# Optimization experiments

Hardware: AMD Instinct MI355X
Metric: run time of the kernel (lower is better)

The kernel has to match this reference:

```python
import jax, jax.numpy as jnp
import numpy as np

N = 50000
E = 800000
IN, H, OUT = 128, 96, 64
BN_EPS = 1e-5


def setup_inputs() -> dict:
    key = jax.random.key(0)
    ks = jax.random.split(key, 16)
    x = jax.random.normal(ks[0], (N, IN), dtype=jnp.float32)
    edge_index = jax.random.randint(ks[1], (2, E), 0, N, dtype=jnp.int64)
    edge_weight = jax.random.uniform(ks[2], (E,), dtype=jnp.float32)
    def lin(k, fo, fi):
        # PyG glorot-ish init
        s = 1.0 / np.sqrt(fi)
        return jax.random.uniform(k, (fo, fi), minval=-s, maxval=s, dtype=jnp.float32)
    W1, b1 = lin(ks[3], H, IN), jnp.zeros((H,), jnp.float32)
    W2, b2 = lin(ks[4], H, H), jnp.zeros((H,), jnp.float32)
    W3, b3 = lin(ks[5], OUT, H), jnp.zeros((OUT,), jnp.float32)
    g1 = jnp.ones((H,), jnp.float32); beta1 = jnp.zeros((H,), jnp.float32)
    m1 = 0.1 * jax.random.normal(ks[6], (H,), dtype=jnp.float32)
    v1 = jnp.abs(1.0 + 0.1 * jax.random.normal(ks[7], (H,), dtype=jnp.float32))
    g2 = jnp.ones((H,), jnp.float32); beta2 = jnp.zeros((H,), jnp.float32)
    m2 = 0.1 * jax.random.normal(ks[8], (H,), dtype=jnp.float32)
    v2 = jnp.abs(1.0 + 0.1 * jax.random.normal(ks[9], (H,), dtype=jnp.float32))
    return dict(x=x, edge_index=edge_index, edge_weight=edge_weight,
                W1=W1, b1=b1, W2=W2, b2=b2, W3=W3, b3=b3,
                g1=g1, beta1=beta1, m1=m1, v1=v1,
                g2=g2, beta2=beta2, m2=m2, v2=v2)


def gcn_norm(edge_index, edge_weight, n):
    # PyG gcn_norm with add_self_loops=True, fill_value=1.0
    loop = jnp.arange(n, dtype=edge_index.dtype)
    row = jnp.concatenate([edge_index[0], loop])  # sources
    col = jnp.concatenate([edge_index[1], loop])  # targets
    ew = jnp.concatenate([edge_weight, jnp.ones((n,), edge_weight.dtype)])
    deg = jax.ops.segment_sum(ew, col, num_segments=n)
    dis = jnp.where(deg > 0, jax.lax.rsqrt(deg), 0.0)  # inf -> 0 masked_fill
    norm = dis[row] * ew * dis[col]
    return row, col, norm


def gcn_conv(x, row, col, norm, W, b, n):
    xw = x @ W.T                       # [N, F_out] dense transform first
    msg = norm[:, None] * xw[row]      # [E+N, F_out] gather + edge scale
    out = jax.ops.segment_sum(msg, col, num_segments=n)  # scatter-add
    return out + b


def bn_eval(x, gamma, beta, mean, var):
    return (x - mean) * jax.lax.rsqrt(var + BN_EPS) * gamma + beta


def reference(x, edge_index, edge_weight, W1, b1, W2, b2, W3, b3,
              g1, beta1, m1, v1, g2, beta2, m2, v2):
    n = x.shape[0]
    row, col, norm = gcn_norm(edge_index, edge_weight, n)  # cached=True: shared
    h = gcn_conv(x, row, col, norm, W1, b1, n)
    h = jax.nn.relu(bn_eval(h, g1, beta1, m1, v1))
    h = gcn_conv(h, row, col, norm, W2, b2, n)
    h = jax.nn.relu(bn_eval(h, g2, beta2, m2, v2))
    out = gcn_conv(h, row, col, norm, W3, b3, n)
    return out
```

## Files before the change

### kernel.cpp

```cpp
#include <hip/hip_runtime.h>
#include <hip/hip_fp16.h>


constexpr float BN_EPS = 1e-5f;
constexpr float FIXED_SCALE = 33554432.0f;
constexpr float INV_FIXED_SCALE = 1.0f / 33554432.0f;
constexpr float NORM_SCALE = 32768.0f;
constexpr float INV_NORM_SCALE = 1.0f / 32768.0f;

typedef _Float16 f16x8 __attribute__((ext_vector_type(8)));
typedef float f32x4 __attribute__((ext_vector_type(4)));


template <int K, int F, bool F32X, bool F32W>
__device__ __forceinline__ void gemm_body(const void* __restrict__ Xin,
                                          const void* __restrict__ Win,
                                          _Float16* __restrict__ Y, int n,
                                          int bid, int tid) {
    constexpr int KT = K / 32;
    constexpr int FT = F / 16;
    int wave = tid >> 6;
    int lane = tid & 63;
    int n0 = (bid * 4 + wave) * 16;
    if (n0 >= n) return;
    int quad = lane >> 4;
    int r = lane & 15;

    f16x8 a[KT];
    if (F32X) {
        const float* xr = (const float*)Xin + (size_t)(n0 + r) * K + quad * 8;
#pragma unroll
        for (int kt = 0; kt < KT; ++kt) {
            float4 v0 = *(const float4*)(xr + kt * 32);
            float4 v1 = *(const float4*)(xr + kt * 32 + 4);
            f16x8 t = {(_Float16)v0.x, (_Float16)v0.y, (_Float16)v0.z, (_Float16)v0.w,
                       (_Float16)v1.x, (_Float16)v1.y, (_Float16)v1.z, (_Float16)v1.w};
            a[kt] = t;
        }
    } else {
        const f16x8* xr = (const f16x8*)((const _Float16*)Xin + (size_t)(n0 + r) * K + quad * 8);
#pragma unroll
        for (int kt = 0; kt < KT; ++kt) a[kt] = xr[kt * 4];
    }

    f32x4 acc[FT];
#pragma unroll
    for (int ft = 0; ft < FT; ++ft) acc[ft] = (f32x4){0.f, 0.f, 0.f, 0.f};

#pragma unroll
    for (int kt = 0; kt < KT; ++kt) {
#pragma unroll
        for (int ft = 0; ft < FT; ++ft) {
            f16x8 b;
            if (F32W) {
                const float* wr = (const float*)Win + (size_t)(ft * 16 + r) * K + kt * 32 + quad * 8;
                float4 v0 = *(const float4*)wr;
                float4 v1 = *(const float4*)(wr + 4);
                f16x8 t = {(_Float16)v0.x, (_Float16)v0.y, (_Float16)v0.z, (_Float16)v0.w,
                           (_Float16)v1.x, (_Float16)v1.y, (_Float16)v1.z, (_Float16)v1.w};
                b = t;
            } else {
                b = *(const f16x8*)((const _Float16*)Win + (size_t)(ft * 16 + r) * K + kt * 32 + quad * 8);
            }
            acc[ft] = __builtin_amdgcn_mfma_f32_16x16x32_f16(a[kt], b, acc[ft], 0, 0, 0);
        }
    }

#pragma unroll
    for (int ft = 0; ft < FT; ++ft) {
#pragma unroll
        for (int reg = 0; reg < 4; ++reg) {
            int row = n0 + quad * 4 + reg;
            Y[(size_t)row * F + ft * 16 + r] = (_Float16)acc[ft][reg];
        }
    }
}

template <int K, int F>
__global__ __launch_bounds__(256) void k_gemm(const _Float16* __restrict__ X,
                                              const _Float16* __restrict__ Wh,
                                              _Float16* __restrict__ Y, int n) {
    gemm_body<K, F, false, false>(X, Wh, Y, n, blockIdx.x, threadIdx.x);
}


__global__ __launch_bounds__(256) void k_mega(
    const int* __restrict__ col_idx, const float* __restrict__ ew,
    unsigned long long* packed, int* rank, int e_cnt, int deg_b,
    const float* __restrict__ x, const float* __restrict__ W1,
    _Float16* __restrict__ bufA, int n, int gg,
    const float* __restrict__ W2, const float* __restrict__ W3,
    _Float16* __restrict__ w2h, _Float16* __restrict__ w3h,
    int w2n4, int w3n4) {
    int b = blockIdx.x;
    if (b < deg_b) {
        int e = b * 256 + threadIdx.x;
        if (e < e_cnt) {
            int c = col_idx[e];
            unsigned int wfix = (unsigned int)(ew[e] * FIXED_SCALE + 0.5f);
            unsigned long long inc = (1ull << 32) | (unsigned long long)wfix;
            unsigned long long old = atomicAdd(&packed[c], inc);
            rank[e] = (int)(old >> 32);
        }
    } else if (b < deg_b + gg) {
        gemm_body<128, 96, true, true>(x, W1, bufA, n, b - deg_b, threadIdx.x);
    } else {
        int i = (b - deg_b - gg) * 256 + threadIdx.x;
        const float* src;
        _Float16* dst;
        int off;
        if (i < w2n4) { src = W2; dst = w2h; off = i; }
        else if (i < w2n4 + w3n4) { src = W3; dst = w3h; off = i - w2n4; }
        else return;
        float4 v = ((const float4*)src)[off];
        __half2 h0 = __floats2half2_rn(v.x, v.y);
        __half2 h1 = __floats2half2_rn(v.z, v.w);
        *(uint2*)(dst + (size_t)off * 4) = make_uint2(*(unsigned*)&h0, *(unsigned*)&h1);
    }
}


__global__ void k_scan1(const unsigned long long* __restrict__ packed,
                        int* bsum, float* dis, int n) {
    __shared__ int s[256];
    int i = blockIdx.x * 256 + threadIdx.x;
    int cnt = 0;
    if (i < n) {
        unsigned long long p = packed[i];
        cnt = (int)(p >> 32);
        float wsum = (float)(unsigned int)(p & 0xffffffffull) * INV_FIXED_SCALE;
        dis[i] = rsqrtf(1.0f + wsum);
    }
    s[threadIdx.x] = cnt;
    __syncthreads();
    for (int off = 128; off > 0; off >>= 1) {
        if (threadIdx.x < off) s[threadIdx.x] += s[threadIdx.x + off];
        __syncthreads();
    }
    if (threadIdx.x == 0) bsum[blockIdx.x] = s[0];
}

__global__ void k_scan23(const unsigned long long* __restrict__ packed,
                         const int* __restrict__ bsum,
                         int* row_ptr, int n, int e_total, int nb) {
    __shared__ int sb[256];
    __shared__ int s[256];
    int t = threadIdx.x;
    int bv = (t < nb) ? bsum[t] : 0;
    sb[t] = bv;
    __syncthreads();
    for (int off = 1; off < 256; off <<= 1) {
        int x = (t >= off) ? sb[t - off] : 0;
        __syncthreads();
        sb[t] += x;
        __syncthreads();
    }
    int boff = (blockIdx.x == 0) ? 0 : sb[blockIdx.x - 1];

    int i = blockIdx.x * 256 + t;
    int v = (i < n) ? (int)(packed[i] >> 32) : 0;
    s[t] = v;
    __syncthreads();
    for (int off = 1; off < 256; off <<= 1) {
        int x = (t >= off) ? s[t - off] : 0;
        __syncthreads();
        s[t] += x;
        __syncthreads();
    }
    int ex = s[t] - v + boff;
    if (i < n) row_ptr[i] = ex;
    if (i == 0) row_ptr[n] = e_total;
}

__global__ void k_fill(const int* __restrict__ row_idx, const int* __restrict__ col_idx,
                       const float* __restrict__ ew, const float* __restrict__ dis,
                       const int* __restrict__ row_ptr, const int* __restrict__ rank,
                       unsigned* ep, int e_cnt) {
    int e = blockIdx.x * 256 + threadIdx.x;
    if (e < e_cnt) {
        int r = row_idx[e];
        int c = col_idx[e];
        float nm = dis[r] * ew[e] * dis[c];
        unsigned q = (unsigned)(nm * NORM_SCALE + 0.5f);
        if (q > 65535u) q = 65535u;
        int p = row_ptr[c] + rank[e];
        ep[p] = ((unsigned)r << 16) | q;
    }
}


__device__ inline void h8_acc(uint4 u, float w, float acc[8]) {
    float2 a = __half22float2(*(const __half2*)&u.x);
    float2 b = __half22float2(*(const __half2*)&u.y);
    float2 c = __half22float2(*(const __half2*)&u.z);
    float2 d = __half22float2(*(const __half2*)&u.w);
    acc[0] = fmaf(w, a.x, acc[0]); acc[1] = fmaf(w, a.y, acc[1]);
    acc[2] = fmaf(w, b.x, acc[2]); acc[3] = fmaf(w, b.y, acc[3]);
    acc[4] = fmaf(w, c.x, acc[4]); acc[5] = fmaf(w, c.y, acc[5]);
    acc[6] = fmaf(w, d.x, acc[6]); acc[7] = fmaf(w, d.y, acc[7]);
}

template <int F, bool BN, bool F32OUT>
__global__ __launch_bounds__(256) void k_aggr(
    const _Float16* __restrict__ xw, const int* __restrict__ row_ptr,
    const unsigned* __restrict__ ep,
    const float* __restrict__ dis, const float* __restrict__ bias,
    const float* __restrict__ g, const float* __restrict__ beta,
    const float* __restrict__ m, const float* __restrict__ v,
    void* __restrict__ out, int n) {
    constexpr int FQ = F / 8;
    int tg = blockIdx.x * 256 + threadIdx.x;
    int node = tg / FQ;
    int q = tg - node * FQ;
    if (node >= n) return;

    const uint4* __restrict__ base = (const uint4*)xw;

    float acc[8];
    {
        float d = dis[node];
        float d2 = d * d;
        uint4 sv = base[(size_t)node * FQ + q];
        float t[8];
        h8_acc(sv, d2, (float*)memset(t, 0, sizeof(t)));
#pragma unroll
        for (int j = 0; j < 8; ++j) acc[j] = t[j];
    }

    int e0 = row_ptr[node], e1 = row_ptr[node + 1];
    int e = e0;
    for (; e + 4 <= e1; e += 4) {
        unsigned p0 = ep[e + 0], p1 = ep[e + 1], p2 = ep[e + 2], p3 = ep[e + 3];
        uint4 x0 = base[(size_t)(p0 >> 16) * FQ + q];
        uint4 x1 = base[(size_t)(p1 >> 16) * FQ + q];
        uint4 x2 = base[(size_t)(p2 >> 16) * FQ + q];
        uint4 x3 = base[(size_t)(p3 >> 16) * FQ + q];
        h8_acc(x0, (float)(p0 & 0xffffu) * INV_NORM_SCALE, acc);
        h8_acc(x1, (float)(p1 & 0xffffu) * INV_NORM_SCALE, acc);
        h8_acc(x2, (float)(p2 & 0xffffu) * INV_NORM_SCALE, acc);
        h8_acc(x3, (float)(p3 & 0xffffu) * INV_NORM_SCALE, acc);
    }
    for (; e < e1; ++e) {
        unsigned p = ep[e];
        uint4 xv = base[(size_t)(p >> 16) * FQ + q];
        h8_acc(xv, (float)(p & 0xffffu) * INV_NORM_SCALE, acc);
    }

    int fb = q * 8;
    const float4* bb = (const float4*)(bias + fb);
    float4 b0 = bb[0], b1 = bb[1];
    acc[0] += b0.x; acc[1] += b0.y; acc[2] += b0.z; acc[3] += b0.w;
    acc[4] += b1.x; acc[5] += b1.y; acc[6] += b1.z; acc[7] += b1.w;
    if (BN) {
        const float* gp = g + fb;
        const float* bp = beta + fb;
        const float* mp = m + fb;
        const float* vp = v + fb;
#pragma unroll
        for (int j = 0; j < 8; ++j) {
            acc[j] = fmaxf((acc[j] - mp[j]) * rsqrtf(vp[j] + BN_EPS) * gp[j] + bp[j], 0.f);
        }
    }
    if (F32OUT) {
        float* op = (float*)out + (size_t)node * F + fb;
        *(float4*)(op + 0) = make_float4(acc[0], acc[1], acc[2], acc[3]);
        *(float4*)(op + 4) = make_float4(acc[4], acc[5], acc[6], acc[7]);
    } else {
        __half2 h0 = __floats2half2_rn(acc[0], acc[1]);
        __half2 h1 = __floats2half2_rn(acc[2], acc[3]);
        __half2 h2 = __floats2half2_rn(acc[4], acc[5]);
        __half2 h3 = __floats2half2_rn(acc[6], acc[7]);
        uint4 u = make_uint4(*(unsigned*)&h0, *(unsigned*)&h1,
                             *(unsigned*)&h2, *(unsigned*)&h3);
        ((uint4*)out)[(size_t)node * FQ + q] = u;
    }
}


extern "C" void kernel_launch(void* const* d_in, const int* in_sizes, int n_in,
                              void* d_out, int out_size, void* d_ws, size_t ws_size,
                              hipStream_t stream) {
    constexpr int IN = 128, H = 96, OUT = 64;

    const float* x   = (const float*)d_in[0];
    const int*   ei  = (const int*)d_in[1];
    const float* ew  = (const float*)d_in[2];
    const float* W1  = (const float*)d_in[3];
    const float* b1  = (const float*)d_in[4];
    const float* W2  = (const float*)d_in[5];
    const float* b2  = (const float*)d_in[6];
    const float* W3  = (const float*)d_in[7];
    const float* b3  = (const float*)d_in[8];
    const float* g1  = (const float*)d_in[9];
    const float* be1 = (const float*)d_in[10];
    const float* m1  = (const float*)d_in[11];
    const float* v1  = (const float*)d_in[12];
    const float* g2  = (const float*)d_in[13];
    const float* be2 = (const float*)d_in[14];
    const float* m2  = (const float*)d_in[15];
    const float* v2  = (const float*)d_in[16];

    const int N = in_sizes[0] / IN;
    const int E = in_sizes[2];
    const int* row_idx = ei;
    const int* col_idx = ei + E;

    char* ws = (char*)d_ws;
    size_t off = 0;
    auto alloc = [&](size_t bytes) -> void* {
        void* p = ws + off;
        off = (off + bytes + 255) & ~(size_t)255;
        return p;
    };
    unsigned long long* packed = (unsigned long long*)alloc((size_t)N * 8);
    float*     dis     = (float*)alloc((size_t)N * 4);
    int*       row_ptr = (int*)alloc((size_t)(N + 1) * 4);
    int*       bsum    = (int*)alloc(256 * 4);
    int*       rank    = (int*)alloc((size_t)E * 4);
    unsigned*  ep      = (unsigned*)alloc((size_t)E * 4);
    _Float16*  w2h     = (_Float16*)alloc((size_t)H * H * 2);
    _Float16*  w3h     = (_Float16*)alloc((size_t)OUT * H * 2);
    _Float16*  bufA    = (_Float16*)alloc((size_t)N * H * 2);
    _Float16*  bufB    = (_Float16*)alloc((size_t)N * H * 2);
    (void)ws_size; (void)n_in; (void)out_size;

    constexpr int W2N4 = H * H / 4, W3N4 = OUT * H / 4;
    const int NB = (N + 255) / 256;
    const int DEG_B = (E + 255) / 256;
    const int GG = (N / 16 + 3) / 4;
    const int CVT_B = (W2N4 + W3N4 + 255) / 256;

    hipMemsetAsync(packed, 0, (size_t)N * 8, stream);
    k_mega<<<DEG_B + GG + CVT_B, 256, 0, stream>>>(
        col_idx, ew, packed, rank, E, DEG_B,
        x, W1, bufA, N, GG, W2, W3, w2h, w3h, W2N4, W3N4);
    k_scan1<<<NB, 256, 0, stream>>>(packed, bsum, dis, N);
    k_scan23<<<NB, 256, 0, stream>>>(packed, bsum, row_ptr, N, E, NB);
    k_fill<<<DEG_B, 256, 0, stream>>>(row_idx, col_idx, ew, dis, row_ptr, rank, ep, E);

    const int GA96 = ((size_t)N * (H / 8) + 255) / 256;
    const int GA64 = ((size_t)N * (OUT / 8) + 255) / 256;

    k_aggr<H, true, false><<<GA96, 256, 0, stream>>>(
        bufA, row_ptr, ep, dis, b1, g1, be1, m1, v1, bufB, N);

    k_gemm<H, H><<<GG, 256, 0, stream>>>(bufB, w2h, bufA, N);
    k_aggr<H, true, false><<<GA96, 256, 0, stream>>>(
        bufA, row_ptr, ep, dis, b2, g2, be2, m2, v2, bufB, N);

    k_gemm<H, OUT><<<GG, 256, 0, stream>>>(bufB, w3h, bufA, N);
    k_aggr<OUT, false, true><<<GA64, 256, 0, stream>>>(
        bufA, row_ptr, ep, dis, b3, nullptr, nullptr, nullptr, nullptr, d_out, N);
}
```

Measured before the change: 281.4 us.

## Fuse all GCN stages into one persistent cooperative kernel with grid syncs

```diff
diff --git a/kernel.cpp b/kernel.cpp
--- a/kernel.cpp
+++ b/kernel.cpp
@@ -1,5 +1,8 @@
 #include <hip/hip_runtime.h>
 #include <hip/hip_fp16.h>
+#include <hip/hip_cooperative_groups.h>
+
+namespace cg = cooperative_groups;
 
 
 constexpr float BN_EPS = 1e-5f;
@@ -11,17 +14,28 @@
 typedef _Float16 f16x8 __attribute__((ext_vector_type(8)));
 typedef float f32x4 __attribute__((ext_vector_type(4)));
 
+struct P {
+    const int* col_idx; const int* row_idx; const float* ew;
+    const float* x; const float* W1; const float* W2; const float* W3;
+    const float* b1; const float* g1; const float* be1; const float* m1; const float* v1;
+    const float* b2; const float* g2; const float* be2; const float* m2; const float* v2;
+    const float* b3;
+    unsigned long long* packed;
+    int* rank; int* row_ptr; int* bsum;
+    float* dis; unsigned* ep;
+    _Float16* w2h; _Float16* w3h; _Float16* bufA; _Float16* bufB;
+    float* out;
+    int N, E, NB;
+};
+
 
 template <int K, int F, bool F32X, bool F32W>
-__device__ __forceinline__ void gemm_body(const void* __restrict__ Xin,
+__device__ __forceinline__ void gemm_wave(const void* __restrict__ Xin,
                                           const void* __restrict__ Win,
-                                          _Float16* __restrict__ Y, int n,
-                                          int bid, int tid) {
+                                          _Float16* __restrict__ Y,
+                                          int n0, int lane, int n) {
     constexpr int KT = K / 32;
     constexpr int FT = F / 16;
-    int wave = tid >> 6;
-    int lane = tid & 63;
-    int n0 = (bid * 4 + wave) * 16;
     if (n0 >= n) return;
     int quad = lane >> 4;
     int r = lane & 15;
@@ -76,118 +90,14 @@
     }
 }
 
-template <int K, int F>
-__global__ __launch_bounds__(256) void k_gemm(const _Float16* __restrict__ X,
-                                              const _Float16* __restrict__ Wh,
-                                              _Float16* __restrict__ Y, int n) {
-    gemm_body<K, F, false, false>(X, Wh, Y, n, blockIdx.x, threadIdx.x);
-}
-
-
-__global__ __launch_bounds__(256) void k_mega(
-    const int* __restrict__ col_idx, const float* __restrict__ ew,
-    unsigned long long* packed, int* rank, int e_cnt, int deg_b,
-    const float* __restrict__ x, const float* __restrict__ W1,
-    _Float16* __restrict__ bufA, int n, int gg,
-    const float* __restrict__ W2, const float* __restrict__ W3,
-    _Float16* __restrict__ w2h, _Float16* __restrict__ w3h,
-    int w2n4, int w3n4) {
-    int b = blockIdx.x;
-    if (b < deg_b) {
-        int e = b * 256 + threadIdx.x;
-        if (e < e_cnt) {
-            int c = col_idx[e];
-            unsigned int wfix = (unsigned int)(ew[e] * FIXED_SCALE + 0.5f);
-            unsigned long long inc = (1ull << 32) | (unsigned long long)wfix;
-            unsigned long long old = atomicAdd(&packed[c], inc);
-            rank[e] = (int)(old >> 32);
-        }
-    } else if (b < deg_b + gg) {
-        gemm_body<128, 96, true, true>(x, W1, bufA, n, b - deg_b, threadIdx.x);
-    } else {
-        int i = (b - deg_b - gg) * 256 + threadIdx.x;
-        const float* src;
-        _Float16* dst;
-        int off;
-        if (i < w2n4) { src = W2; dst = w2h; off = i; }
-        else if (i < w2n4 + w3n4) { src = W3; dst = w3h; off = i - w2n4; }
-        else return;
-        float4 v = ((const float4*)src)[off];
-        __half2 h0 = __floats2half2_rn(v.x, v.y);
-        __half2 h1 = __floats2half2_rn(v.z, v.w);
-        *(uint2*)(dst + (size_t)off * 4) = make_uint2(*(unsigned*)&h0, *(unsigned*)&h1);
-    }
-}
-
-
-__global__ void k_scan1(const unsigned long long* __restrict__ packed,
-                        int* bsum, float* dis, int n) {
-    __shared__ int s[256];
-    int i = blockIdx.x * 256 + threadIdx.x;
-    int cnt = 0;
-    if (i < n) {
-        unsigned long long p = packed[i];
-        cnt = (int)(p >> 32);
-        float wsum = (float)(unsigned int)(p & 0xffffffffull) * INV_FIXED_SCALE;
-        dis[i] = rsqrtf(1.0f + wsum);
-    }
-    s[threadIdx.x] = cnt;
-    __syncthreads();
-    for (int off = 128; off > 0; off >>= 1) {
-        if (threadIdx.x < off) s[threadIdx.x] += s[threadIdx.x + off];
-        __syncthreads();
-    }
-    if (threadIdx.x == 0) bsum[blockIdx.x] = s[0];
-}
-
-__global__ void k_scan23(const unsigned long long* __restrict__ packed,
-                         const int* __restrict__ bsum,
-                         int* row_ptr, int n, int e_total, int nb) {
-    __shared__ int sb[256];
-    __shared__ int s[256];
-    int t = threadIdx.x;
-    int bv = (t < nb) ? bsum[t] : 0;
-    sb[t] = bv;
-    __syncthreads();
-    for (int off = 1; off < 256; off <<= 1) {
-        int x = (t >= off) ? sb[t - off] : 0;
-        __syncthreads();
-        sb[t] += x;
-        __syncthreads();
-    }
-    int boff = (blockIdx.x == 0) ? 0 : sb[blockIdx.x - 1];
-
-    int i = blockIdx.x * 256 + t;
-    int v = (i < n) ? (int)(packed[i] >> 32) : 0;
-    s[t] = v;
-    __syncthreads();
-    for (int off = 1; off < 256; off <<= 1) {
-        int x = (t >= off) ? s[t - off] : 0;
-        __syncthreads();
-        s[t] += x;
-        __syncthreads();
-    }
-    int ex = s[t] - v + boff;
-    if (i < n) row_ptr[i] = ex;
-    if (i == 0) row_ptr[n] = e_total;
-}
-
-__global__ void k_fill(const int* __restrict__ row_idx, const int* __restrict__ col_idx,
-                       const float* __restrict__ ew, const float* __restrict__ dis,
-                       const int* __restrict__ row_ptr, const int* __restrict__ rank,
-                       unsigned* ep, int e_cnt) {
-    int e = blockIdx.x * 256 + threadIdx.x;
-    if (e < e_cnt) {
-        int r = row_idx[e];
-        int c = col_idx[e];
-        float nm = dis[r] * ew[e] * dis[c];
-        unsigned q = (unsigned)(nm * NORM_SCALE + 0.5f);
-        if (q > 65535u) q = 65535u;
-        int p = row_ptr[c] + rank[e];
-        ep[p] = ((unsigned)r << 16) | q;
-    }
-}
-
+
+__device__ inline void cvt8(uint4 u, float* f) {
+    float2 t;
+    t = __half22float2(*(const __half2*)&u.x); f[0] = t.x; f[1] = t.y;
+    t = __half22float2(*(const __half2*)&u.y); f[2] = t.x; f[3] = t.y;
+    t = __half22float2(*(const __half2*)&u.z); f[4] = t.x; f[5] = t.y;
+    t = __half22float2(*(const __half2*)&u.w); f[6] = t.x; f[7] = t.y;
+}
 
 __device__ inline void h8_acc(uint4 u, float w, float acc[8]) {
     float2 a = __half22float2(*(const __half2*)&u.x);
@@ -201,79 +111,198 @@
 }
 
 template <int F, bool BN, bool F32OUT>
-__global__ __launch_bounds__(256) void k_aggr(
-    const _Float16* __restrict__ xw, const int* __restrict__ row_ptr,
-    const unsigned* __restrict__ ep,
-    const float* __restrict__ dis, const float* __restrict__ bias,
-    const float* __restrict__ g, const float* __restrict__ beta,
-    const float* __restrict__ m, const float* __restrict__ v,
-    void* __restrict__ out, int n) {
+__device__ void aggr_phase(const _Float16* __restrict__ xw,
+                           const int* __restrict__ row_ptr,
+                           const unsigned* __restrict__ ep,
+                           const float* __restrict__ dis,
+                           const float* __restrict__ bias,
+                           const float* __restrict__ g, const float* __restrict__ beta,
+                           const float* __restrict__ m, const float* __restrict__ v,
+                           void* __restrict__ out, int n, int tid, int gsz) {
     constexpr int FQ = F / 8;
-    int tg = blockIdx.x * 256 + threadIdx.x;
-    int node = tg / FQ;
-    int q = tg - node * FQ;
-    if (node >= n) return;
-
     const uint4* __restrict__ base = (const uint4*)xw;
-
-    float acc[8];
-    {
-        float d = dis[node];
-        float d2 = d * d;
-        uint4 sv = base[(size_t)node * FQ + q];
-        float t[8];
-        h8_acc(sv, d2, (float*)memset(t, 0, sizeof(t)));
-#pragma unroll
-        for (int j = 0; j < 8; ++j) acc[j] = t[j];
-    }
-
-    int e0 = row_ptr[node], e1 = row_ptr[node + 1];
-    int e = e0;
-    for (; e + 4 <= e1; e += 4) {
-        unsigned p0 = ep[e + 0], p1 = ep[e + 1], p2 = ep[e + 2], p3 = ep[e + 3];
-        uint4 x0 = base[(size_t)(p0 >> 16) * FQ + q];
-        uint4 x1 = base[(size_t)(p1 >> 16) * FQ + q];
-        uint4 x2 = base[(size_t)(p2 >> 16) * FQ + q];
-        uint4 x3 = base[(size_t)(p3 >> 16) * FQ + q];
-        h8_acc(x0, (float)(p0 & 0xffffu) * INV_NORM_SCALE, acc);
-        h8_acc(x1, (float)(p1 & 0xffffu) * INV_NORM_SCALE, acc);
-        h8_acc(x2, (float)(p2 & 0xffffu) * INV_NORM_SCALE, acc);
-        h8_acc(x3, (float)(p3 & 0xffffu) * INV_NORM_SCALE, acc);
-    }
-    for (; e < e1; ++e) {
-        unsigned p = ep[e];
-        uint4 xv = base[(size_t)(p >> 16) * FQ + q];
-        h8_acc(xv, (float)(p & 0xffffu) * INV_NORM_SCALE, acc);
-    }
-
-    int fb = q * 8;
-    const float4* bb = (const float4*)(bias + fb);
-    float4 b0 = bb[0], b1 = bb[1];
-    acc[0] += b0.x; acc[1] += b0.y; acc[2] += b0.z; acc[3] += b0.w;
-    acc[4] += b1.x; acc[5] += b1.y; acc[6] += b1.z; acc[7] += b1.w;
-    if (BN) {
-        const float* gp = g + fb;
-        const float* bp = beta + fb;
-        const float* mp = m + fb;
-        const float* vp = v + fb;
-#pragma unroll
-        for (int j = 0; j < 8; ++j) {
-            acc[j] = fmaxf((acc[j] - mp[j]) * rsqrtf(vp[j] + BN_EPS) * gp[j] + bp[j], 0.f);
-        }
-    }
-    if (F32OUT) {
-        float* op = (float*)out + (size_t)node * F + fb;
-        *(float4*)(op + 0) = make_float4(acc[0], acc[1], acc[2], acc[3]);
-        *(float4*)(op + 4) = make_float4(acc[4], acc[5], acc[6], acc[7]);
+    int total = n * FQ;
+    for (int it = tid; it < total; it += gsz) {
+        int node = it / FQ;
+        int q = it - node * FQ;
+
+        float acc[8];
+        {
+            float d = dis[node];
+            float d2 = d * d;
+            uint4 sv = base[(size_t)node * FQ + q];
+            float t[8];
+            cvt8(sv, t);
+#pragma unroll
+            for (int j = 0; j < 8; ++j) acc[j] = d2 * t[j];
+        }
+
+        int e0 = row_ptr[node], e1 = row_ptr[node + 1];
+        int e = e0;
+        for (; e + 4 <= e1; e += 4) {
+            unsigned p0 = ep[e + 0], p1 = ep[e + 1], p2 = ep[e + 2], p3 = ep[e + 3];
+            uint4 x0 = base[(size_t)(p0 >> 16) * FQ + q];
+            uint4 x1 = base[(size_t)(p1 >> 16) * FQ + q];
+            uint4 x2 = base[(size_t)(p2 >> 16) * FQ + q];
+            uint4 x3 = base[(size_t)(p3 >> 16) * FQ + q];
+            h8_acc(x0, (float)(p0 & 0xffffu) * INV_NORM_SCALE, acc);
+            h8_acc(x1, (float)(p1 & 0xffffu) * INV_NORM_SCALE, acc);
+            h8_acc(x2, (float)(p2 & 0xffffu) * INV_NORM_SCALE, acc);
+            h8_acc(x3, (float)(p3 & 0xffffu) * INV_NORM_SCALE, acc);
+        }
+        for (; e < e1; ++e) {
+            unsigned p = ep[e];
+            uint4 xv = base[(size_t)(p >> 16) * FQ + q];
+            h8_acc(xv, (float)(p & 0xffffu) * INV_NORM_SCALE, acc);
+        }
+
+        int fb = q * 8;
+        const float4* bb = (const float4*)(bias + fb);
+        float4 b0 = bb[0], b1 = bb[1];
+        acc[0] += b0.x; acc[1] += b0.y; acc[2] += b0.z; acc[3] += b0.w;
+        acc[4] += b1.x; acc[5] += b1.y; acc[6] += b1.z; acc[7] += b1.w;
+        if (BN) {
+#pragma unroll
+            for (int j = 0; j < 8; ++j) {
+                acc[j] = fmaxf((acc[j] - m[fb + j]) * rsqrtf(v[fb + j] + BN_EPS) * g[fb + j]
+                               + beta[fb + j], 0.f);
+            }
+        }
+        if (F32OUT) {
+            float* op = (float*)out + (size_t)node * F + fb;
+            *(float4*)(op + 0) = make_float4(acc[0], acc[1], acc[2], acc[3]);
+            *(float4*)(op + 4) = make_float4(acc[4], acc[5], acc[6], acc[7]);
+        } else {
+            __half2 h0 = __floats2half2_rn(acc[0], acc[1]);
+            __half2 h1 = __floats2half2_rn(acc[2], acc[3]);
+            __half2 h2 = __floats2half2_rn(acc[4], acc[5]);
+            __half2 h3 = __floats2half2_rn(acc[6], acc[7]);
+            uint4 u = make_uint4(*(unsigned*)&h0, *(unsigned*)&h1,
+                                 *(unsigned*)&h2, *(unsigned*)&h3);
+            ((uint4*)out)[(size_t)node * FQ + q] = u;
+        }
+    }
+}
+
+
+__global__ __launch_bounds__(256, 4) void k_all(P p) {
+    cg::grid_group grid = cg::this_grid();
+    const int nB = (int)gridDim.x;
+    const int gsz = nB * 256;
+    const int tid = (int)blockIdx.x * 256 + (int)threadIdx.x;
+    const int wave = threadIdx.x >> 6;
+    const int lane = threadIdx.x & 63;
+    const int tiles = p.N / 16;
+    constexpr int W2N4 = 96 * 96 / 4, W3N4 = 64 * 96 / 4;
+
+    for (int i = tid; i < p.N; i += gsz) p.packed[i] = 0ull;
+    grid.sync();
+
+    if (wave == 0) {
+        int chunk = (p.E + nB - 1) / nB;
+        int e0 = (int)blockIdx.x * chunk;
+        int e1 = min(e0 + chunk, p.E);
+        for (int e = e0 + lane; e < e1; e += 64) {
+            int c = p.col_idx[e];
+            unsigned wfix = (unsigned)(p.ew[e] * FIXED_SCALE + 0.5f);
+            unsigned long long inc = (1ull << 32) | (unsigned long long)wfix;
+            unsigned long long old = atomicAdd(&p.packed[c], inc);
+            p.rank[e] = (int)(old >> 32);
+        }
+        int i = (int)blockIdx.x * 64 + lane;
+        if (i < W2N4 + W3N4) {
+            const float* src; _Float16* dst; int o;
+            if (i < W2N4) { src = p.W2; dst = p.w2h; o = i; }
+            else          { src = p.W3; dst = p.w3h; o = i - W2N4; }
+            float4 vv = ((const float4*)src)[o];
+            __half2 h0 = __floats2half2_rn(vv.x, vv.y);
+            __half2 h1 = __floats2half2_rn(vv.z, vv.w);
+            *(uint2*)(dst + (size_t)o * 4) = make_uint2(*(unsigned*)&h0, *(unsigned*)&h1);
+        }
     } else {
-        __half2 h0 = __floats2half2_rn(acc[0], acc[1]);
-        __half2 h1 = __floats2half2_rn(acc[2], acc[3]);
-        __half2 h2 = __floats2half2_rn(acc[4], acc[5]);
-        __half2 h3 = __floats2half2_rn(acc[6], acc[7]);
-        uint4 u = make_uint4(*(unsigned*)&h0, *(unsigned*)&h1,
-                             *(unsigned*)&h2, *(unsigned*)&h3);
-        ((uint4*)out)[(size_t)node * FQ + q] = u;
-    }
+        for (int t = (int)blockIdx.x * 3 + (wave - 1); t < tiles; t += 3 * nB)
+            gemm_wave<128, 96, true, true>(p.x, p.W1, p.bufA, t * 16, lane, p.N);
+    }
+    grid.sync();
+
+    if ((int)blockIdx.x < p.NB) {
+        __shared__ int s1[256];
+        int i = (int)blockIdx.x * 256 + (int)threadIdx.x;
+        int cnt = 0;
+        if (i < p.N) {
+            unsigned long long pk = p.packed[i];
+            cnt = (int)(pk >> 32);
+            float wsum = (float)(unsigned)(pk & 0xffffffffull) * INV_FIXED_SCALE;
+            p.dis[i] = rsqrtf(1.0f + wsum);
+        }
+        s1[threadIdx.x] = cnt;
+        __syncthreads();
+        for (int off = 128; off > 0; off >>= 1) {
+            if ((int)threadIdx.x < off) s1[threadIdx.x] += s1[threadIdx.x + off];
+            __syncthreads();
+        }
+        if (threadIdx.x == 0) p.bsum[blockIdx.x] = s1[0];
+    }
+    grid.sync();
+
+    if ((int)blockIdx.x < p.NB) {
+        __shared__ int sb[256];
+        __shared__ int s2[256];
+        int t = threadIdx.x;
+        int bv = (t < p.NB) ? p.bsum[t] : 0;
+        sb[t] = bv;
+        __syncthreads();
+        for (int off = 1; off < 256; off <<= 1) {
+            int xx = (t >= off) ? sb[t - off] : 0;
+            __syncthreads();
+            sb[t] += xx;
+            __syncthreads();
+        }
+        int boff = (blockIdx.x == 0) ? 0 : sb[blockIdx.x - 1];
+        int i = (int)blockIdx.x * 256 + t;
+        int v = (i < p.N) ? (int)(p.packed[i] >> 32) : 0;
+        s2[t] = v;
+        __syncthreads();
+        for (int off = 1; off < 256; off <<= 1) {
+            int xx = (t >= off) ? s2[t - off] : 0;
+            __syncthreads();
+            s2[t] += xx;
+            __syncthreads();
+        }
+        int ex = s2[t] - v + boff;
+        if (i < p.N) p.row_ptr[i] = ex;
+        if (i == 0) p.row_ptr[p.N] = p.E;
+    }
+    grid.sync();
+
+    for (int e = tid; e < p.E; e += gsz) {
+        int r = p.row_idx[e];
+        int c = p.col_idx[e];
+        float nm = p.dis[r] * p.ew[e] * p.dis[c];
+        unsigned q = (unsigned)(nm * NORM_SCALE + 0.5f);
+        if (q > 65535u) q = 65535u;
+        p.ep[p.row_ptr[c] + p.rank[e]] = ((unsigned)r << 16) | q;
+    }
+    grid.sync();
+
+    aggr_phase<96, true, false>(p.bufA, p.row_ptr, p.ep, p.dis, p.b1,
+                                p.g1, p.be1, p.m1, p.v1, p.bufB, p.N, tid, gsz);
+    grid.sync();
+
+    for (int t = (int)blockIdx.x * 4 + wave; t < tiles; t += 4 * nB)
+        gemm_wave<96, 96, false, false>(p.bufB, p.w2h, p.bufA, t * 16, lane, p.N);
+    grid.sync();
+
+    aggr_phase<96, true, false>(p.bufA, p.row_ptr, p.ep, p.dis, p.b2,
+                                p.g2, p.be2, p.m2, p.v2, p.bufB, p.N, tid, gsz);
+    grid.sync();
+
+    for (int t = (int)blockIdx.x * 4 + wave; t < tiles; t += 4 * nB)
+        gemm_wave<96, 64, false, false>(p.bufB, p.w3h, p.bufA, t * 16, lane, p.N);
+    grid.sync();
+
+    aggr_phase<64, false, true>(p.bufA, p.row_ptr, p.ep, p.dis, p.b3,
+                                nullptr, nullptr, nullptr, nullptr, p.out, p.N, tid, gsz);
 }
 
 
@@ -282,28 +311,8 @@
                               hipStream_t stream) {
     constexpr int IN = 128, H = 96, OUT = 64;
 
-    const float* x   = (const float*)d_in[0];
-    const int*   ei  = (const int*)d_in[1];
-    const float* ew  = (const float*)d_in[2];
-    const float* W1  = (const float*)d_in[3];
-    const float* b1  = (const float*)d_in[4];
-    const float* W2  = (const float*)d_in[5];
-    const float* b2  = (const float*)d_in[6];
-    const float* W3  = (const float*)d_in[7];
-    const float* b3  = (const float*)d_in[8];
-    const float* g1  = (const float*)d_in[9];
-    const float* be1 = (const float*)d_in[10];
-    const float* m1  = (const float*)d_in[11];
-    const float* v1  = (const float*)d_in[12];
-    const float* g2  = (const float*)d_in[13];
-    const float* be2 = (const float*)d_in[14];
-    const float* m2  = (const float*)d_in[15];
-    const float* v2  = (const float*)d_in[16];
-
     const int N = in_sizes[0] / IN;
     const int E = in_sizes[2];
-    const int* row_idx = ei;
-    const int* col_idx = ei + E;
 
     char* ws = (char*)d_ws;
     size_t off = 0;
@@ -312,43 +321,42 @@
         off = (off + bytes + 255) & ~(size_t)255;
         return p;
     };
-    unsigned long long* packed = (unsigned long long*)alloc((size_t)N * 8);
-    float*     dis     = (float*)alloc((size_t)N * 4);
-    int*       row_ptr = (int*)alloc((size_t)(N + 1) * 4);
-    int*       bsum    = (int*)alloc(256 * 4);
-    int*       rank    = (int*)alloc((size_t)E * 4);
-    unsigned*  ep      = (unsigned*)alloc((size_t)E * 4);
-    _Float16*  w2h     = (_Float16*)alloc((size_t)H * H * 2);
-    _Float16*  w3h     = (_Float16*)alloc((size_t)OUT * H * 2);
-    _Float16*  bufA    = (_Float16*)alloc((size_t)N * H * 2);
-    _Float16*  bufB    = (_Float16*)alloc((size_t)N * H * 2);
+
+    P prm;
+    prm.col_idx = (const int*)d_in[1] + E;
+    prm.row_idx = (const int*)d_in[1];
+    prm.ew  = (const float*)d_in[2];
+    prm.x   = (const float*)d_in[0];
+    prm.W1  = (const float*)d_in[3];  prm.b1 = (const float*)d_in[4];
+    prm.W2  = (const float*)d_in[5];  prm.b2 = (const float*)d_in[6];
+    prm.W3  = (const float*)d_in[7];  prm.b3 = (const float*)d_in[8];
+    prm.g1  = (const float*)d_in[9];  prm.be1 = (const float*)d_in[10];
+    prm.m1  = (const float*)d_in[11]; prm.v1  = (const float*)d_in[12];
+    prm.g2  = (const float*)d_in[13]; prm.be2 = (const float*)d_in[14];
+    prm.m2  = (const float*)d_in[15]; prm.v2  = (const float*)d_in[16];
+
+    prm.packed  = (unsigned long long*)alloc((size_t)N * 8);
+    prm.dis     = (float*)alloc((size_t)N * 4);
+    prm.row_ptr = (int*)alloc((size_t)(N + 1) * 4);
+    prm.bsum    = (int*)alloc(256 * 4);
+    prm.rank    = (int*)alloc((size_t)E * 4);
+    prm.ep      = (unsigned*)alloc((size_t)E * 4);
+    prm.w2h     = (_Float16*)alloc((size_t)H * H * 2);
+    prm.w3h     = (_Float16*)alloc((size_t)OUT * H * 2);
+    prm.bufA    = (_Float16*)alloc((size_t)N * H * 2);
+    prm.bufB    = (_Float16*)alloc((size_t)N * H * 2);
+    prm.out     = (float*)d_out;
+    prm.N = N; prm.E = E; prm.NB = (N + 255) / 256;
     (void)ws_size; (void)n_in; (void)out_size;
 
-    constexpr int W2N4 = H * H / 4, W3N4 = OUT * H / 4;
-    const int NB = (N + 255) / 256;
-    const int DEG_B = (E + 255) / 256;
-    const int GG = (N / 16 + 3) / 4;
-    const int CVT_B = (W2N4 + W3N4 + 255) / 256;
-
-    hipMemsetAsync(packed, 0, (size_t)N * 8, stream);
-    k_mega<<<DEG_B + GG + CVT_B, 256, 0, stream>>>(
-        col_idx, ew, packed, rank, E, DEG_B,
-        x, W1, bufA, N, GG, W2, W3, w2h, w3h, W2N4, W3N4);
-    k_scan1<<<NB, 256, 0, stream>>>(packed, bsum, dis, N);
-    k_scan23<<<NB, 256, 0, stream>>>(packed, bsum, row_ptr, N, E, NB);
-    k_fill<<<DEG_B, 256, 0, stream>>>(row_idx, col_idx, ew, dis, row_ptr, rank, ep, E);
-
-    const int GA96 = ((size_t)N * (H / 8) + 255) / 256;
-    const int GA64 = ((size_t)N * (OUT / 8) + 255) / 256;
-
-    k_aggr<H, true, false><<<GA96, 256, 0, stream>>>(
-        bufA, row_ptr, ep, dis, b1, g1, be1, m1, v1, bufB, N);
-
-    k_gemm<H, H><<<GG, 256, 0, stream>>>(bufB, w2h, bufA, N);
-    k_aggr<H, true, false><<<GA96, 256, 0, stream>>>(
-        bufA, row_ptr, ep, dis, b2, g2, be2, m2, v2, bufB, N);
-
-    k_gemm<H, OUT><<<GG, 256, 0, stream>>>(bufB, w3h, bufA, N);
-    k_aggr<OUT, false, true><<<GA64, 256, 0, stream>>>(
-        bufA, row_ptr, ep, dis, b3, nullptr, nullptr, nullptr, nullptr, d_out, N);
-}
+    int perCU = 0;
+    if (hipOccupancyMaxActiveBlocksPerMultiprocessor(&perCU, (const void*)k_all, 256, 0)
+            != hipSuccess || perCU <= 0)
+        perCU = 2;
+    long long nb = (long long)perCU * 256;
+    if (nb > 1024) nb = 1024;
+    if (nb < 256) nb = 256;
+
+    void* args[] = {&prm};
+    hipLaunchCooperativeKernel((void*)k_all, dim3((unsigned)nb), dim3(256), args, 0, stream);
+}
```

Result: slower. 821.5 us (+192.0%).

## Stage GEMM output through LDS and interleave degree-count blocks with W1 GEMM blocks

Applied to the files above, without the earlier changes.

```diff
diff --git a/kernel.cpp b/kernel.cpp
--- a/kernel.cpp
+++ b/kernel.cpp
@@ -13,66 +13,81 @@
 
 
 template <int K, int F, bool F32X, bool F32W>
-__device__ __forceinline__ void gemm_body(const void* __restrict__ Xin,
-                                          const void* __restrict__ Win,
-                                          _Float16* __restrict__ Y, int n,
-                                          int bid, int tid) {
+__device__ __forceinline__ void gemm_block(const void* __restrict__ Xin,
+                                           const void* __restrict__ Win,
+                                           _Float16* __restrict__ Y,
+                                           int n0b, int tid, int n,
+                                           _Float16* lds) {
     constexpr int KT = K / 32;
     constexpr int FT = F / 16;
+    constexpr int LROW = (F == 96) ? 104 : 72;
     int wave = tid >> 6;
     int lane = tid & 63;
-    int n0 = (bid * 4 + wave) * 16;
-    if (n0 >= n) return;
     int quad = lane >> 4;
     int r = lane & 15;
-
-    f16x8 a[KT];
-    if (F32X) {
-        const float* xr = (const float*)Xin + (size_t)(n0 + r) * K + quad * 8;
-#pragma unroll
-        for (int kt = 0; kt < KT; ++kt) {
-            float4 v0 = *(const float4*)(xr + kt * 32);
-            float4 v1 = *(const float4*)(xr + kt * 32 + 4);
-            f16x8 t = {(_Float16)v0.x, (_Float16)v0.y, (_Float16)v0.z, (_Float16)v0.w,
-                       (_Float16)v1.x, (_Float16)v1.y, (_Float16)v1.z, (_Float16)v1.w};
-            a[kt] = t;
-        }
-    } else {
-        const f16x8* xr = (const f16x8*)((const _Float16*)Xin + (size_t)(n0 + r) * K + quad * 8);
-#pragma unroll
-        for (int kt = 0; kt < KT; ++kt) a[kt] = xr[kt * 4];
-    }
-
-    f32x4 acc[FT];
-#pragma unroll
-    for (int ft = 0; ft < FT; ++ft) acc[ft] = (f32x4){0.f, 0.f, 0.f, 0.f};
-
-#pragma unroll
-    for (int kt = 0; kt < KT; ++kt) {
-#pragma unroll
-        for (int ft = 0; ft < FT; ++ft) {
-            f16x8 b;
-            if (F32W) {
-                const float* wr = (const float*)Win + (size_t)(ft * 16 + r) * K + kt * 32 + quad * 8;
-                float4 v0 = *(const float4*)wr;
-                float4 v1 = *(const float4*)(wr + 4);
+    int n0 = n0b + wave * 16;
+    bool active = (n0 < n);
+
+    if (active) {
+        f16x8 a[KT];
+        if (F32X) {
+            const float* xr = (const float*)Xin + (size_t)(n0 + r) * K + quad * 8;
+#pragma unroll
+            for (int kt = 0; kt < KT; ++kt) {
+                float4 v0 = *(const float4*)(xr + kt * 32);
+                float4 v1 = *(const float4*)(xr + kt * 32 + 4);
                 f16x8 t = {(_Float16)v0.x, (_Float16)v0.y, (_Float16)v0.z, (_Float16)v0.w,
                            (_Float16)v1.x, (_Float16)v1.y, (_Float16)v1.z, (_Float16)v1.w};
-                b = t;
-            } else {
-                b = *(const f16x8*)((const _Float16*)Win + (size_t)(ft * 16 + r) * K + kt * 32 + quad * 8);
+                a[kt] = t;
             }
-            acc[ft] = __builtin_amdgcn_mfma_f32_16x16x32_f16(a[kt], b, acc[ft], 0, 0, 0);
-        }
-    }
-
-#pragma unroll
-    for (int ft = 0; ft < FT; ++ft) {
-#pragma unroll
-        for (int reg = 0; reg < 4; ++reg) {
-            int row = n0 + quad * 4 + reg;
-            Y[(size_t)row * F + ft * 16 + r] = (_Float16)acc[ft][reg];
-        }
+        } else {
+            const f16x8* xr = (const f16x8*)((const _Float16*)Xin + (size_t)(n0 + r) * K + quad * 8);
+#pragma unroll
+            for (int kt = 0; kt < KT; ++kt) a[kt] = xr[kt * 4];
+        }
+
+        f32x4 acc[FT];
+#pragma unroll
+        for (int ft = 0; ft < FT; ++ft) acc[ft] = (f32x4){0.f, 0.f, 0.f, 0.f};
+
+#pragma unroll
+        for (int kt = 0; kt < KT; ++kt) {
+#pragma unroll
+            for (int ft = 0; ft < FT; ++ft) {
+                f16x8 b;
+                if (F32W) {
+                    const float* wr = (const float*)Win + (size_t)(ft * 16 + r) * K + kt * 32 + quad * 8;
+                    float4 v0 = *(const float4*)wr;
+                    float4 v1 = *(const float4*)(wr + 4);
+                    f16x8 t = {(_Float16)v0.x, (_Float16)v0.y, (_Float16)v0.z, (_Float16)v0.w,
+                               (_Float16)v1.x, (_Float16)v1.y, (_Float16)v1.z, (_Float16)v1.w};
+                    b = t;
+                } else {
+                    b = *(const f16x8*)((const _Float16*)Win + (size_t)(ft * 16 + r) * K + kt * 32 + quad * 8);
+                }
+                acc[ft] = __builtin_amdgcn_mfma_f32_16x16x32_f16(a[kt], b, acc[ft], 0, 0, 0);
+            }
+        }
+
+#pragma unroll
+        for (int ft = 0; ft < FT; ++ft) {
+#pragma unroll
+            for (int reg = 0; reg < 4; ++reg) {
+                int lr = wave * 16 + quad * 4 + reg;
+                lds[(size_t)lr * LROW + ft * 16 + r] = (_Float16)acc[ft][reg];
+            }
+        }
+    }
+    __syncthreads();
+
+    constexpr int CPR = F / 8;
+    constexpr int TOTAL = 64 * CPR;
+    for (int i = tid; i < TOTAL; i += 256) {
+        int row = i / CPR, c = i - row * CPR;
+        int grow = n0b + row;
+        if (grow < n)
+            *(uint4*)(Y + (size_t)grow * F + c * 8) =
+                *(const uint4*)(lds + (size_t)row * LROW + c * 8);
     }
 }
 
@@ -80,42 +95,48 @@
 __global__ __launch_bounds__(256) void k_gemm(const _Float16* __restrict__ X,
                                               const _Float16* __restrict__ Wh,
                                               _Float16* __restrict__ Y, int n) {
-    gemm_body<K, F, false, false>(X, Wh, Y, n, blockIdx.x, threadIdx.x);
+    __shared__ _Float16 lds[64 * 104];
+    gemm_block<K, F, false, false>(X, Wh, Y, blockIdx.x * 64, threadIdx.x, n, lds);
 }
 
 
 __global__ __launch_bounds__(256) void k_mega(
     const int* __restrict__ col_idx, const float* __restrict__ ew,
-    unsigned long long* packed, int* rank, int e_cnt, int deg_b,
+    unsigned long long* packed, int* rank, int e_cnt, int pair_b,
     const float* __restrict__ x, const float* __restrict__ W1,
-    _Float16* __restrict__ bufA, int n, int gg,
+    _Float16* __restrict__ bufA, int n,
     const float* __restrict__ W2, const float* __restrict__ W3,
     _Float16* __restrict__ w2h, _Float16* __restrict__ w3h,
     int w2n4, int w3n4) {
+    __shared__ _Float16 lds[64 * 104];
     int b = blockIdx.x;
-    if (b < deg_b) {
-        int e = b * 256 + threadIdx.x;
-        if (e < e_cnt) {
-            int c = col_idx[e];
-            unsigned int wfix = (unsigned int)(ew[e] * FIXED_SCALE + 0.5f);
-            unsigned long long inc = (1ull << 32) | (unsigned long long)wfix;
-            unsigned long long old = atomicAdd(&packed[c], inc);
-            rank[e] = (int)(old >> 32);
-        }
-    } else if (b < deg_b + gg) {
-        gemm_body<128, 96, true, true>(x, W1, bufA, n, b - deg_b, threadIdx.x);
+    if (b < 2 * pair_b) {
+        int q = b >> 1;
+        if ((b & 1) == 0) {
+#pragma unroll
+            for (int j = 0; j < 4; ++j) {
+                int e = q * 1024 + j * 256 + (int)threadIdx.x;
+                if (e < e_cnt) {
+                    int c = col_idx[e];
+                    unsigned wfix = (unsigned)(ew[e] * FIXED_SCALE + 0.5f);
+                    unsigned long long inc = (1ull << 32) | (unsigned long long)wfix;
+                    unsigned long long old = atomicAdd(&packed[c], inc);
+                    rank[e] = (int)(old >> 32);
+                }
+            }
+        } else {
+            gemm_block<128, 96, true, true>(x, W1, bufA, q * 64, threadIdx.x, n, lds);
+        }
     } else {
-        int i = (b - deg_b - gg) * 256 + threadIdx.x;
-        const float* src;
-        _Float16* dst;
-        int off;
-        if (i < w2n4) { src = W2; dst = w2h; off = i; }
-        else if (i < w2n4 + w3n4) { src = W3; dst = w3h; off = i - w2n4; }
+        int i = (b - 2 * pair_b) * 256 + (int)threadIdx.x;
+        const float* src; _Float16* dst; int o;
+        if (i < w2n4) { src = W2; dst = w2h; o = i; }
+        else if (i < w2n4 + w3n4) { src = W3; dst = w3h; o = i - w2n4; }
         else return;
-        float4 v = ((const float4*)src)[off];
+        float4 v = ((const float4*)src)[o];
         __half2 h0 = __floats2half2_rn(v.x, v.y);
         __half2 h1 = __floats2half2_rn(v.z, v.w);
-        *(uint2*)(dst + (size_t)off * 4) = make_uint2(*(unsigned*)&h0, *(unsigned*)&h1);
+        *(uint2*)(dst + (size_t)o * 4) = make_uint2(*(unsigned*)&h0, *(unsigned*)&h1);
     }
 }
 
@@ -128,13 +149,13 @@
     if (i < n) {
         unsigned long long p = packed[i];
         cnt = (int)(p >> 32);
-        float wsum = (float)(unsigned int)(p & 0xffffffffull) * INV_FIXED_SCALE;
+        float wsum = (float)(unsigned)(p & 0xffffffffull) * INV_FIXED_SCALE;
         dis[i] = rsqrtf(1.0f + wsum);
     }
     s[threadIdx.x] = cnt;
     __syncthreads();
     for (int off = 128; off > 0; off >>= 1) {
-        if (threadIdx.x < off) s[threadIdx.x] += s[threadIdx.x + off];
+        if ((int)threadIdx.x < off) s[threadIdx.x] += s[threadIdx.x + off];
         __syncthreads();
     }
     if (threadIdx.x == 0) bsum[blockIdx.x] = s[0];
@@ -183,11 +204,18 @@
         float nm = dis[r] * ew[e] * dis[c];
         unsigned q = (unsigned)(nm * NORM_SCALE + 0.5f);
         if (q > 65535u) q = 65535u;
-        int p = row_ptr[c] + rank[e];
-        ep[p] = ((unsigned)r << 16) | q;
-    }
-}
-
+        ep[row_ptr[c] + rank[e]] = ((unsigned)r << 16) | q;
+    }
+}
+
+
+__device__ inline void cvt8(uint4 u, float* f) {
+    float2 t;
+    t = __half22float2(*(const __half2*)&u.x); f[0] = t.x; f[1] = t.y;
+    t = __half22float2(*(const __half2*)&u.y); f[2] = t.x; f[3] = t.y;
+    t = __half22float2(*(const __half2*)&u.z); f[4] = t.x; f[5] = t.y;
+    t = __half22float2(*(const __half2*)&u.w); f[6] = t.x; f[7] = t.y;
+}
 
 __device__ inline void h8_acc(uint4 u, float w, float acc[8]) {
     float2 a = __half22float2(*(const __half2*)&u.x);
@@ -222,9 +250,9 @@
         float d2 = d * d;
         uint4 sv = base[(size_t)node * FQ + q];
         float t[8];
-        h8_acc(sv, d2, (float*)memset(t, 0, sizeof(t)));
-#pragma unroll
-        for (int j = 0; j < 8; ++j) acc[j] = t[j];
+        cvt8(sv, t);
+#pragma unroll
+        for (int j = 0; j < 8; ++j) acc[j] = d2 * t[j];
     }
 
     int e0 = row_ptr[node], e1 = row_ptr[node + 1];
@@ -252,13 +280,10 @@
     acc[0] += b0.x; acc[1] += b0.y; acc[2] += b0.z; acc[3] += b0.w;
     acc[4] += b1.x; acc[5] += b1.y; acc[6] += b1.z; acc[7] += b1.w;
     if (BN) {
-        const float* gp = g + fb;
-        const float* bp = beta + fb;
-        const float* mp = m + fb;
-        const float* vp = v + fb;
 #pragma unroll
         for (int j = 0; j < 8; ++j) {
-            acc[j] = fmaxf((acc[j] - mp[j]) * rsqrtf(vp[j] + BN_EPS) * gp[j] + bp[j], 0.f);
+            acc[j] = fmaxf((acc[j] - m[fb + j]) * rsqrtf(v[fb + j] + BN_EPS) * g[fb + j]
+                           + beta[fb + j], 0.f);
         }
     }
     if (F32OUT) {
@@ -326,17 +351,19 @@
 
     constexpr int W2N4 = H * H / 4, W3N4 = OUT * H / 4;
     const int NB = (N + 255) / 256;
-    const int DEG_B = (E + 255) / 256;
+    const int DEG1024 = (E + 1023) / 1024;
     const int GG = (N / 16 + 3) / 4;
+    const int PAIR = (DEG1024 > GG) ? DEG1024 : GG;
     const int CVT_B = (W2N4 + W3N4 + 255) / 256;
 
     hipMemsetAsync(packed, 0, (size_t)N * 8, stream);
-    k_mega<<<DEG_B + GG + CVT_B, 256, 0, stream>>>(
-        col_idx, ew, packed, rank, E, DEG_B,
-        x, W1, bufA, N, GG, W2, W3, w2h, w3h, W2N4, W3N4);
+    k_mega<<<2 * PAIR + CVT_B, 256, 0, stream>>>(
+        col_idx, ew, packed, rank, E, PAIR,
+        x, W1, bufA, N, W2, W3, w2h, w3h, W2N4, W3N4);
     k_scan1<<<NB, 256, 0, stream>>>(packed, bsum, dis, N);
     k_scan23<<<NB, 256, 0, stream>>>(packed, bsum, row_ptr, N, E, NB);
-    k_fill<<<DEG_B, 256, 0, stream>>>(row_idx, col_idx, ew, dis, row_ptr, rank, ep, E);
+    k_fill<<<(E + 255) / 256, 256, 0, stream>>>(row_idx, col_idx, ew, dis,
+                                                row_ptr, rank, ep, E);
 
     const int GA96 = ((size_t)N * (H / 8) + 255) / 256;
     const int GA64 = ((size_t)N * (OUT / 8) + 255) / 256;
```

After: 264.9 us, median of 2. -5.9%, faster.
